# Optimization experiments

Measured on AMD Instinct MI355X. Metric: run time of the kernel, lower is better.

The kernel has to match this reference:

```python
import jax, jax.numpy as jnp
import numpy as np

B, C, H, W, NH = 4, 96, 256, 256, 4


def setup_inputs() -> dict:
    key = jax.random.key(0)
    ks = jax.random.split(key, 8)
    s = 0.05  # keep pre-activations well-scaled
    return {
        "x": jax.random.normal(ks[0], (B, C, H, W), jnp.float32),
        "ff": jax.random.normal(ks[1], (B, C, H, W), jnp.float32),
        "w_q": jax.random.normal(ks[2], (C, C, 1, 1), jnp.float32) * s,
        "w_kv": jax.random.normal(ks[3], (2 * C, C, 1, 1), jnp.float32) * s,
        "w_q_dw": jax.random.normal(ks[4], (C, 1, 3, 3), jnp.float32) * s,
        "w_kv_dw": jax.random.normal(ks[5], (2 * C, 1, 3, 3), jnp.float32) * s,
        "w_out": jax.random.normal(ks[6], (C, C, 1, 1), jnp.float32) * s,
        "temperature": jnp.ones((NH, 1, 1), jnp.float32),
    }


def _conv1x1(x, w):
    # pointwise conv == channel GEMM; w: [O, I, 1, 1]
    return jnp.einsum('bchw,oc->bohw', x, w[:, :, 0, 0])


def _dwconv3(x, w):
    # depthwise 3x3, padding=1; w: [C, 1, 3, 3]
    return jax.lax.conv_general_dilated(
        x, w, window_strides=(1, 1), padding='SAME',
        feature_group_count=x.shape[1],
        dimension_numbers=('NCHW', 'OIHW', 'NCHW'))


def _l2norm(t, eps=1e-12):
    # L2-normalize along last (HW) axis, torch F.normalize semantics
    n = jnp.sqrt(jnp.sum(t * t, axis=-1, keepdims=True))
    return t / jnp.maximum(n, eps)


def reference(x, ff, w_q, w_kv, w_q_dw, w_kv_dw, w_out, temperature):
    b, c, h, w = x.shape
    q = _dwconv3(_conv1x1(ff, w_q), w_q_dw)          # [B,C,H,W]
    kv = _dwconv3(_conv1x1(x, w_kv), w_kv_dw)        # [B,2C,H,W]
    k, v = jnp.split(kv, 2, axis=1)

    def heads(t):
        return t.reshape(b, NH, c // NH, h * w)       # [B,nh,c,HW]

    q = _l2norm(heads(q))
    k = _l2norm(heads(k))
    v = heads(v)
    # channel-wise (transposed) attention: [B,nh,c,c]
    attn = jax.nn.softmax(jnp.einsum('bhcn,bhdn->bhcd', q, k) * temperature, axis=-1)
    o = jnp.einsum('bhcd,bhdn->bhcn', attn, v).reshape(b, c, h, w)
    return _conv1x1(o, w_out)
```

## Files before the change

kernel.cpp:

```cpp
#include <hip/hip_runtime.h>
#include <hip/hip_bf16.h>
#include <hip/hip_fp16.h>

typedef unsigned int u32;
typedef unsigned short u16;
typedef _Float16 f16;

static constexpr int HWn = 65536;

typedef __attribute__((ext_vector_type(8))) f16 f16x8;
typedef __attribute__((ext_vector_type(4))) float f32x4;

__device__ __forceinline__ float h2f(u16 u) {
    union { u16 s; f16 h; } z; z.s = u; return (float)z.h;
}
__device__ __forceinline__ u16 f2h(float f) {
    union { u16 s; f16 h; } z; z.h = (f16)f; return z.s;
}
__device__ __forceinline__ u32 pack2h(float a, float b) {
    union { u32 i; f16 h[2]; } z; z.h[0] = (f16)a; z.h[1] = (f16)b; return z.i;
}
__device__ __forceinline__ float hlo(u32 u) {
    union { u32 i; f16 h[2]; } z; z.i = u; return (float)z.h[0];
}
__device__ __forceinline__ float hhi(u32 u) {
    union { u32 i; f16 h[2]; } z; z.i = u; return (float)z.h[1];
}
__device__ __forceinline__ float sq2h(u32 a) {
    const float l = hlo(a), h = hhi(a);
    return fmaf(l, l, h * h);
}

__device__ __forceinline__ int xoff(int px, int icb) {
    return px * 128 + (((icb ^ (px & 7) ^ ((px >> 3) & 7))) << 3);
}

__global__ __launch_bounds__(256) void k_prep_w(
    const float* __restrict__ wq, const float* __restrict__ wkv,
    u16* __restrict__ wf)
{
    const int i = blockIdx.x * 256 + threadIdx.x;
    if (i >= 288 * 96) return;
    const int row = i / 96, ic = i % 96;
    const float w = (row < 96) ? wq[row * 96 + ic] : wkv[(row - 96) * 96 + ic];
    wf[i] = f2h(w);
}

__global__ __launch_bounds__(256, 5) void k_conv_mfma(
    const float* __restrict__ ff, const float* __restrict__ x,
    const u16* __restrict__ wf,
    u16* __restrict__ qpre, u16* __restrict__ kvpre)
{
    const int b = blockIdx.z, sec = blockIdx.y;
    const int px0 = blockIdx.x * 128;
    const int tid = threadIdx.x;

    __shared__ __align__(16) u16 xs[16384];

    const float* src = (sec == 0 ? ff : x) + (size_t)b * 96 * HWn;

    const int icq = (tid >> 4) * 2;
    const int pxs = (tid & 15) * 8;
    #pragma unroll 1
    for (int p = 0; p < 3; ++p) {
        const int ic = p * 32 + icq;
        const float* rp0 = src + (size_t)ic * HWn + px0 + pxs;
        const float* rp1 = rp0 + HWn;
        const float4 a0 = *reinterpret_cast<const float4*>(rp0);
        const float4 a1 = *reinterpret_cast<const float4*>(rp0 + 4);
        const float4 b0 = *reinterpret_cast<const float4*>(rp1);
        const float4 b1 = *reinterpret_cast<const float4*>(rp1 + 4);
        const int icb = ic >> 3, icl = ic & 7;
        const float e0[8] = {a0.x, a0.y, a0.z, a0.w, a1.x, a1.y, a1.z, a1.w};
        const float e1[8] = {b0.x, b0.y, b0.z, b0.w, b1.x, b1.y, b1.z, b1.w};
        #pragma unroll
        for (int j = 0; j < 8; ++j) {
            const int o = xoff(pxs + j, icb) + icl;
            *reinterpret_cast<u32*>(&xs[o]) = pack2h(e0[j], e1[j]);
        }
    }
    __syncthreads();

    const int lane = tid & 63;
    const int wv = tid >> 6;
    const int oc0 = (wv >> 1) * 48;
    const int pxw = (wv & 1) * 64;
    const int lr = lane & 15, lg = lane >> 4;

    const int npass = (sec == 0) ? 1 : 2;
    #pragma unroll 1
    for (int kvs = 0; kvs < npass; ++kvs) {
        const u16* wh = wf + ((sec == 0) ? 0 : (96 + kvs * 96)) * 96;
        u16* dst = (sec == 0) ? (qpre + (size_t)b * 96 * HWn)
                              : (kvpre + (size_t)b * 192 * HWn + (size_t)kvs * 96 * HWn);

        f32x4 acc[3][4];
        #pragma unroll
        for (int m = 0; m < 3; ++m)
            #pragma unroll
            for (int n = 0; n < 4; ++n)
                acc[m][n] = (f32x4){0.f, 0.f, 0.f, 0.f};

        #pragma unroll 1
        for (int kt = 0; kt < 3; ++kt) {
            const int kb = kt * 32;
            f16x8 B[4];
            #pragma unroll
            for (int n = 0; n < 4; ++n)
                B[n] = *(const f16x8*)(xs + xoff(pxw + n * 16 + lr, (kb >> 3) + lg));
            f16x8 A[3];
            #pragma unroll
            for (int m = 0; m < 3; ++m)
                A[m] = *(const f16x8*)(wh + (oc0 + m * 16 + lr) * 96 + kb + lg * 8);
            #pragma unroll
            for (int m = 0; m < 3; ++m)
                #pragma unroll
                for (int n = 0; n < 4; ++n)
                    acc[m][n] = __builtin_amdgcn_mfma_f32_16x16x32_f16(A[m], B[n], acc[m][n], 0, 0, 0);
        }

        #pragma unroll
        for (int m = 0; m < 3; ++m) {
            #pragma unroll
            for (int i = 0; i < 4; ++i) {
                const int oc = oc0 + m * 16 + lg * 4 + i;
                u16* drow = dst + (size_t)oc * HWn + px0;
                #pragma unroll
                for (int n = 0; n < 4; ++n)
                    drow[pxw + n * 16 + lr] = f2h(acc[m][n][i]);
            }
        }
    }
}

__global__ __launch_bounds__(512) void k_dw_fused(
    const u16* __restrict__ qpre, const u16* __restrict__ kvpre,
    const float* __restrict__ wqdw, const float* __restrict__ wkvdw,
    u16* __restrict__ vout, float* __restrict__ ssq, float* __restrict__ Sg)
{
    const int bid = blockIdx.x;
    const int wg = (bid & 7) * 256 + (bid >> 3);
    const int b = wg >> 9;
    const int rem = wg & 511;
    const int y = rem >> 1;
    const int tx = (rem & 1) * 128;
    const int tid = threadIdx.x;
    const int lane = tid & 63;
    const int chunk = tid & 15;
    const int x0l = chunk * 8;
    const int xg = tx + x0l;

    __shared__ __align__(16) u16 qs[96][136];
    __shared__ __align__(16) u16 ks[96][136];

    #pragma unroll 1
    for (int it = 0; it < 9; ++it) {
        const int p = it * 32 + (tid >> 4);
        const u16* src; const float* wp; int c;
        if (p < 96)       { c = p;       src = qpre  + ((size_t)(b * 96 + c)) * HWn;       wp = wqdw  + c * 9; }
        else if (p < 192) { c = p - 96;  src = kvpre + ((size_t)(b * 192 + c)) * HWn;      wp = wkvdw + c * 9; }
        else              { c = p - 192; src = kvpre + ((size_t)(b * 192 + 96 + c)) * HWn; wp = wkvdw + (96 + c) * 9; }

        float a0 = 0.f, a1 = 0.f, a2 = 0.f, a3 = 0.f, a4 = 0.f, a5 = 0.f, a6 = 0.f, a7 = 0.f;

        #pragma unroll
        for (int r = 0; r < 3; ++r) {
            const int ry = y + r - 1;
            if ((unsigned)ry < 256u) {
                const u16* row = src + ry * 256 + xg;
                const uint4 m = *reinterpret_cast<const uint4*>(row);
                const float v1 = hlo(m.x), v2 = hhi(m.x);
                const float v3 = hlo(m.y), v4 = hhi(m.y);
                const float v5 = hlo(m.z), v6 = hhi(m.z);
                const float v7 = hlo(m.w), v8 = hhi(m.w);
                const float lv = __shfl(v8, (lane - 1) & 63);
                const float rv = __shfl(v1, (lane + 1) & 63);
                const float v0 = (chunk == 0)  ? ((xg > 0)       ? h2f(row[-1]) : 0.f) : lv;
                const float v9 = (chunk == 15) ? ((xg + 8 < 256) ? h2f(row[8])  : 0.f) : rv;
                const float w0 = wp[r * 3 + 0], w1 = wp[r * 3 + 1], w2 = wp[r * 3 + 2];
                a0 = fmaf(w0, v0, fmaf(w1, v1, fmaf(w2, v2, a0)));
                a1 = fmaf(w0, v1, fmaf(w1, v2, fmaf(w2, v3, a1)));
                a2 = fmaf(w0, v2, fmaf(w1, v3, fmaf(w2, v4, a2)));
                a3 = fmaf(w0, v3, fmaf(w1, v4, fmaf(w2, v5, a3)));
                a4 = fmaf(w0, v4, fmaf(w1, v5, fmaf(w2, v6, a4)));
                a5 = fmaf(w0, v5, fmaf(w1, v6, fmaf(w2, v7, a5)));
                a6 = fmaf(w0, v6, fmaf(w1, v7, fmaf(w2, v8, a6)));
                a7 = fmaf(w0, v7, fmaf(w1, v8, fmaf(w2, v9, a7)));
            }
        }

        const uint4 o = make_uint4(pack2h(a0, a1), pack2h(a2, a3), pack2h(a4, a5), pack2h(a6, a7));
        if (p < 96) {
            *reinterpret_cast<uint4*>(&qs[c][x0l]) = o;
        } else if (p < 192) {
            *reinterpret_cast<uint4*>(&ks[c][x0l]) = o;
        } else {
            *reinterpret_cast<uint4*>(vout + ((size_t)(b * 96 + c)) * HWn + y * 256 + xg) = o;
        }
    }
    __syncthreads();

    if (tid < 384) {
        const int half = tid >= 192;
        const int r = tid - half * 192;
        const uint4* rr = reinterpret_cast<const uint4*>(
            (r < 96 ? &qs[r][0] : &ks[r - 96][0]) + half * 64);
        float s = 0.f;
        #pragma unroll
        for (int pch = 0; pch < 8; ++pch) {
            const uint4 a = rr[pch];
            s += sq2h(a.x) + sq2h(a.y) + sq2h(a.z) + sq2h(a.w);
        }
        atomicAdd(ssq + b * 192 + r, s);
    }

    {
        const int w = tid >> 6;
        const int h = w & 3, mt = w >> 2;
        const int lr2 = lane & 15, lg2 = lane >> 4;
        const int ar = h * 24 + min(mt * 16 + lr2, 23);
        f32x4 acc2[2];
        acc2[0] = (f32x4){0.f, 0.f, 0.f, 0.f};
        acc2[1] = (f32x4){0.f, 0.f, 0.f, 0.f};
        #pragma unroll
        for (int ks4 = 0; ks4 < 4; ++ks4) {
            const f16x8 A = *(const f16x8*)(&qs[ar][ks4 * 32 + lg2 * 8]);
            #pragma unroll
            for (int nt = 0; nt < 2; ++nt) {
                const int bc = h * 24 + min(nt * 16 + lr2, 23);
                const f16x8 B = *(const f16x8*)(&ks[bc][ks4 * 32 + lg2 * 8]);
                acc2[nt] = __builtin_amdgcn_mfma_f32_16x16x32_f16(A, B, acc2[nt], 0, 0, 0);
            }
        }
        #pragma unroll
        for (int nt = 0; nt < 2; ++nt) {
            const int col = nt * 16 + lr2;
            #pragma unroll
            for (int reg = 0; reg < 4; ++reg) {
                const int row24 = mt * 16 + lg2 * 4 + reg;
                if (row24 < 24 && col < 24)
                    atomicAdd(Sg + b * 2304 + h * 576 + row24 * 24 + col, acc2[nt][reg]);
            }
        }
    }
}

__global__ __launch_bounds__(256) void k_attn_fold(
    const float* __restrict__ ssq, const float* __restrict__ S,
    const float* __restrict__ temp, const float* __restrict__ w_out,
    u16* __restrict__ mf)
{
    const int b = blockIdx.x;
    const int tid = threadIdx.x;
    __shared__ float rq[96], rk[96], att[2304];

    if (tid < 96) {
        rq[tid] = 1.f / fmaxf(sqrtf(ssq[b * 192 + tid]), 1e-12f);
    } else if (tid < 192) {
        const int c = tid - 96;
        rk[c] = 1.f / fmaxf(sqrtf(ssq[b * 192 + 96 + c]), 1e-12f);
    }
    __syncthreads();

    if (tid < 96) {
        const int h = tid / 24, i = tid % 24;
        const float tmp = temp[h];
        const float rqi = rq[h * 24 + i];
        float l[24];
        float m = -1e30f;
        #pragma unroll
        for (int j = 0; j < 24; ++j) {
            l[j] = S[b * 2304 + (h * 24 + i) * 24 + j] * rqi * rk[h * 24 + j] * tmp;
            m = fmaxf(m, l[j]);
        }
        float ssum = 0.f;
        #pragma unroll
        for (int j = 0; j < 24; ++j) { l[j] = expf(l[j] - m); ssum += l[j]; }
        const float inv = 1.f / ssum;
        #pragma unroll
        for (int j = 0; j < 24; ++j) att[(h * 24 + i) * 24 + j] = l[j] * inv;
    }
    __syncthreads();

    for (int k = 0; k < 36; ++k) {
        const int id = k * 256 + tid;
        const int dg = id / 96, oc = id % 96;
        const int h = dg / 24, d24 = dg % 24;
        float s = 0.f;
        #pragma unroll
        for (int i = 0; i < 24; ++i) {
            s += w_out[oc * 96 + h * 24 + i] * att[(h * 24 + i) * 24 + d24];
        }
        mf[b * 9216 + oc * 96 + dg] = f2h(s);
    }
}

__global__ __launch_bounds__(256, 5) void k_out_mfma(
    const u16* __restrict__ v, const u16* __restrict__ mf,
    float* __restrict__ out)
{
    const int b = blockIdx.y;
    const int px0 = blockIdx.x * 128;
    const int tid = threadIdx.x;
    __shared__ __align__(16) u16 xt[16384];

    const u16* vb = v + (size_t)b * 96 * HWn;
    const u16* mh = mf + b * 9216;

    const int icq = (tid >> 4) * 2;
    const int pxs = (tid & 15) * 8;
    #pragma unroll 1
    for (int p = 0; p < 3; ++p) {
        const int dg = p * 32 + icq;
        const uint4 u0 = *reinterpret_cast<const uint4*>(vb + (size_t)dg * HWn + px0 + pxs);
        const uint4 u1 = *reinterpret_cast<const uint4*>(vb + (size_t)(dg + 1) * HWn + px0 + pxs);
        const u32 w0[4] = {u0.x, u0.y, u0.z, u0.w};
        const u32 w1[4] = {u1.x, u1.y, u1.z, u1.w};
        const int icb = dg >> 3, icl = dg & 7;
        #pragma unroll
        for (int j = 0; j < 8; ++j) {
            const u32 lo = (w0[j >> 1] >> ((j & 1) * 16)) & 0xffffu;
            const u32 hi = (w1[j >> 1] >> ((j & 1) * 16)) & 0xffffu;
            const int o = xoff(pxs + j, icb) + icl;
            *reinterpret_cast<u32*>(&xt[o]) = (hi << 16) | lo;
        }
    }
    __syncthreads();

    const int lane = tid & 63;
    const int wv = tid >> 6;
    const int oc0 = (wv >> 1) * 48;
    const int pxw = (wv & 1) * 64;
    const int lr = lane & 15, lg = lane >> 4;

    f32x4 acc[3][4];
    #pragma unroll
    for (int m = 0; m < 3; ++m)
        #pragma unroll
        for (int n = 0; n < 4; ++n)
            acc[m][n] = (f32x4){0.f, 0.f, 0.f, 0.f};

    #pragma unroll 1
    for (int kt = 0; kt < 3; ++kt) {
        const int kb = kt * 32;
        f16x8 B[4];
        #pragma unroll
        for (int n = 0; n < 4; ++n)
            B[n] = *(const f16x8*)(xt + xoff(pxw + n * 16 + lr, (kb >> 3) + lg));
        f16x8 A[3];
        #pragma unroll
        for (int m = 0; m < 3; ++m)
            A[m] = *(const f16x8*)(mh + (oc0 + m * 16 + lr) * 96 + kb + lg * 8);
        #pragma unroll
        for (int m = 0; m < 3; ++m)
            #pragma unroll
            for (int n = 0; n < 4; ++n)
                acc[m][n] = __builtin_amdgcn_mfma_f32_16x16x32_f16(A[m], B[n], acc[m][n], 0, 0, 0);
    }

    #pragma unroll
    for (int m = 0; m < 3; ++m) {
        #pragma unroll
        for (int i = 0; i < 4; ++i) {
            const int oc = oc0 + m * 16 + lg * 4 + i;
            float* drow = out + ((size_t)(b * 96 + oc)) * HWn + px0;
            #pragma unroll
            for (int n = 0; n < 4; ++n)
                drow[pxw + n * 16 + lr] = acc[m][n][i];
        }
    }
}

extern "C" void kernel_launch(void* const* d_in, const int* in_sizes, int n_in,
                              void* d_out, int out_size, void* d_ws, size_t ws_size,
                              hipStream_t stream) {
    (void)in_sizes; (void)n_in; (void)out_size; (void)ws_size;
    const float* x      = (const float*)d_in[0];
    const float* ff     = (const float*)d_in[1];
    const float* w_q    = (const float*)d_in[2];
    const float* w_kv   = (const float*)d_in[3];
    const float* w_q_dw = (const float*)d_in[4];
    const float* w_kv_dw= (const float*)d_in[5];
    const float* w_out  = (const float*)d_in[6];
    const float* temp   = (const float*)d_in[7];
    float* out = (float*)d_out;

    char* ws = (char*)d_ws;
    u16* qpre   = (u16*)(ws);
    u16* kvpre  = (u16*)(ws + 50331648);
    u16* vbuf   = (u16*)(ws + 150994944);
    float* ssq  = (float*)(ws + 201326592);
    float* S    = (float*)(ws + 201329664);
    u16* wf     = (u16*)(ws + 201366528);
    u16* mf     = (u16*)(ws + 201421824);

    hipMemsetAsync(ssq, 0, 3072 + 36864, stream);

    k_prep_w<<<108, 256, 0, stream>>>(w_q, w_kv, wf);
    k_conv_mfma<<<dim3(512, 2, 4), 256, 0, stream>>>(ff, x, wf, qpre, kvpre);
    k_dw_fused<<<dim3(2048), 512, 0, stream>>>(qpre, kvpre, w_q_dw, w_kv_dw, vbuf, ssq, S);
    k_attn_fold<<<4, 256, 0, stream>>>(ssq, S, temp, w_out, mf);
    k_out_mfma<<<dim3(512, 4), 256, 0, stream>>>(vbuf, mf, out);
}
```

Before: 275.4 us.

## Prefetch depthwise rows, spread atomic reductions over partial copies, unroll staging loops

The depthwise kernel now issues the global loads for the next channel before computing the current one, with boundary handling folded into predicated loads. This is meant to hide load latency. Atomic accumulation of squared norms and Q·K scores is spread across 32 partial buffers indexed by block, to cut contention on the same addresses. The attention-fold kernel then sums those partials. Load-staging loops in the conv and output kernels are also fully unrolled. The trade-off is higher register pressure, a larger memset, and extra reduction work in the fold kernel.

```diff
diff --git a/kernel.cpp b/kernel.cpp
--- a/kernel.cpp
+++ b/kernel.cpp
@@ -7,6 +7,7 @@
 typedef _Float16 f16;
 
 static constexpr int HWn = 65536;
+static constexpr int NCOPY = 32;
 
 typedef __attribute__((ext_vector_type(8))) f16 f16x8;
 typedef __attribute__((ext_vector_type(4))) float f32x4;
@@ -61,7 +62,7 @@
 
     const int icq = (tid >> 4) * 2;
     const int pxs = (tid & 15) * 8;
-    #pragma unroll 1
+    #pragma unroll
     for (int p = 0; p < 3; ++p) {
         const int ic = p * 32 + icq;
         const float* rp0 = src + (size_t)ic * HWn + px0 + pxs;
@@ -133,69 +134,106 @@
     }
 }
 
+__device__ __forceinline__ void dw_addr(
+    int it, int pq, int b,
+    const u16* qpre, const u16* kvpre, const float* wqdw, const float* wkvdw,
+    const u16*& src, const float*& wp, int& c, int& seg)
+{
+    const int p = it * 32 + pq;
+    if (p < 96)       { c = p;       src = qpre  + ((size_t)(b * 96 + c)) * HWn;       wp = wqdw  + c * 9; seg = 0; }
+    else if (p < 192) { c = p - 96;  src = kvpre + ((size_t)(b * 192 + c)) * HWn;      wp = wkvdw + c * 9; seg = 1; }
+    else              { c = p - 192; src = kvpre + ((size_t)(b * 192 + 96 + c)) * HWn; wp = wkvdw + (96 + c) * 9; seg = 2; }
+}
+
 __global__ __launch_bounds__(512) void k_dw_fused(
     const u16* __restrict__ qpre, const u16* __restrict__ kvpre,
     const float* __restrict__ wqdw, const float* __restrict__ wkvdw,
-    u16* __restrict__ vout, float* __restrict__ ssq, float* __restrict__ Sg)
+    u16* __restrict__ vout, float* __restrict__ ssqp, float* __restrict__ Spart)
 {
     const int bid = blockIdx.x;
     const int wg = (bid & 7) * 256 + (bid >> 3);
+    const int copy = bid & (NCOPY - 1);
     const int b = wg >> 9;
     const int rem = wg & 511;
     const int y = rem >> 1;
     const int tx = (rem & 1) * 128;
     const int tid = threadIdx.x;
     const int lane = tid & 63;
+    const int pq = tid >> 4;
     const int chunk = tid & 15;
     const int x0l = chunk * 8;
     const int xg = tx + x0l;
 
+    const bool vr0 = (y > 0), vr2 = (y < 255);
+    const bool le = (chunk == 0) && (xg > 0);
+    const bool re = (chunk == 15) && (xg + 8 < 256);
+
     __shared__ __align__(16) u16 qs[96][136];
     __shared__ __align__(16) u16 ks[96][136];
 
+    auto issue = [&](const u16* src, uint4* m, u32* el, u32* er) {
+        const uint4 z = make_uint4(0u, 0u, 0u, 0u);
+        const u16* r0 = src + (y - 1) * 256 + xg;
+        const u16* r1 = r0 + 256;
+        const u16* r2 = r1 + 256;
+        m[0] = vr0 ? *reinterpret_cast<const uint4*>(r0) : z;
+        m[1] = *reinterpret_cast<const uint4*>(r1);
+        m[2] = vr2 ? *reinterpret_cast<const uint4*>(r2) : z;
+        el[0] = (le && vr0) ? r0[-1] : 0u;  er[0] = (re && vr0) ? r0[8] : 0u;
+        el[1] = le ? r1[-1] : 0u;           er[1] = re ? r1[8] : 0u;
+        el[2] = (le && vr2) ? r2[-1] : 0u;  er[2] = (re && vr2) ? r2[8] : 0u;
+    };
+
+    const u16* srcC; const float* wpC; int cC, segC;
+    dw_addr(0, pq, b, qpre, kvpre, wqdw, wkvdw, srcC, wpC, cC, segC);
+    uint4 mcur[3]; u32 elc[3], erc[3];
+    issue(srcC, mcur, elc, erc);
+
     #pragma unroll 1
     for (int it = 0; it < 9; ++it) {
-        const int p = it * 32 + (tid >> 4);
-        const u16* src; const float* wp; int c;
-        if (p < 96)       { c = p;       src = qpre  + ((size_t)(b * 96 + c)) * HWn;       wp = wqdw  + c * 9; }
-        else if (p < 192) { c = p - 96;  src = kvpre + ((size_t)(b * 192 + c)) * HWn;      wp = wkvdw + c * 9; }
-        else              { c = p - 192; src = kvpre + ((size_t)(b * 192 + 96 + c)) * HWn; wp = wkvdw + (96 + c) * 9; }
+        const u16* srcN; const float* wpN; int cN, segN;
+        uint4 mnx[3]; u32 eln[3], ern[3];
+        if (it < 8) {
+            dw_addr(it + 1, pq, b, qpre, kvpre, wqdw, wkvdw, srcN, wpN, cN, segN);
+            issue(srcN, mnx, eln, ern);
+        }
 
         float a0 = 0.f, a1 = 0.f, a2 = 0.f, a3 = 0.f, a4 = 0.f, a5 = 0.f, a6 = 0.f, a7 = 0.f;
-
         #pragma unroll
         for (int r = 0; r < 3; ++r) {
-            const int ry = y + r - 1;
-            if ((unsigned)ry < 256u) {
-                const u16* row = src + ry * 256 + xg;
-                const uint4 m = *reinterpret_cast<const uint4*>(row);
-                const float v1 = hlo(m.x), v2 = hhi(m.x);
-                const float v3 = hlo(m.y), v4 = hhi(m.y);
-                const float v5 = hlo(m.z), v6 = hhi(m.z);
-                const float v7 = hlo(m.w), v8 = hhi(m.w);
-                const float lv = __shfl(v8, (lane - 1) & 63);
-                const float rv = __shfl(v1, (lane + 1) & 63);
-                const float v0 = (chunk == 0)  ? ((xg > 0)       ? h2f(row[-1]) : 0.f) : lv;
-                const float v9 = (chunk == 15) ? ((xg + 8 < 256) ? h2f(row[8])  : 0.f) : rv;
-                const float w0 = wp[r * 3 + 0], w1 = wp[r * 3 + 1], w2 = wp[r * 3 + 2];
-                a0 = fmaf(w0, v0, fmaf(w1, v1, fmaf(w2, v2, a0)));
-                a1 = fmaf(w0, v1, fmaf(w1, v2, fmaf(w2, v3, a1)));
-                a2 = fmaf(w0, v2, fmaf(w1, v3, fmaf(w2, v4, a2)));
-                a3 = fmaf(w0, v3, fmaf(w1, v4, fmaf(w2, v5, a3)));
-                a4 = fmaf(w0, v4, fmaf(w1, v5, fmaf(w2, v6, a4)));
-                a5 = fmaf(w0, v5, fmaf(w1, v6, fmaf(w2, v7, a5)));
-                a6 = fmaf(w0, v6, fmaf(w1, v7, fmaf(w2, v8, a6)));
-                a7 = fmaf(w0, v7, fmaf(w1, v8, fmaf(w2, v9, a7)));
-            }
+            const uint4 m = mcur[r];
+            const float v1 = hlo(m.x), v2 = hhi(m.x);
+            const float v3 = hlo(m.y), v4 = hhi(m.y);
+            const float v5 = hlo(m.z), v6 = hhi(m.z);
+            const float v7 = hlo(m.w), v8 = hhi(m.w);
+            const float lv = __shfl(v8, (lane - 1) & 63);
+            const float rv = __shfl(v1, (lane + 1) & 63);
+            const float v0 = (chunk == 0)  ? h2f((u16)elc[r]) : lv;
+            const float v9 = (chunk == 15) ? h2f((u16)erc[r]) : rv;
+            const float w0 = wpC[r * 3 + 0], w1 = wpC[r * 3 + 1], w2 = wpC[r * 3 + 2];
+            a0 = fmaf(w0, v0, fmaf(w1, v1, fmaf(w2, v2, a0)));
+            a1 = fmaf(w0, v1, fmaf(w1, v2, fmaf(w2, v3, a1)));
+            a2 = fmaf(w0, v2, fmaf(w1, v3, fmaf(w2, v4, a2)));
+            a3 = fmaf(w0, v3, fmaf(w1, v4, fmaf(w2, v5, a3)));
+            a4 = fmaf(w0, v4, fmaf(w1, v5, fmaf(w2, v6, a4)));
+            a5 = fmaf(w0, v5, fmaf(w1, v6, fmaf(w2, v7, a5)));
+            a6 = fmaf(w0, v6, fmaf(w1, v7, fmaf(w2, v8, a6)));
+            a7 = fmaf(w0, v7, fmaf(w1, v8, fmaf(w2, v9, a7)));
         }
 
         const uint4 o = make_uint4(pack2h(a0, a1), pack2h(a2, a3), pack2h(a4, a5), pack2h(a6, a7));
-        if (p < 96) {
-            *reinterpret_cast<uint4*>(&qs[c][x0l]) = o;
-        } else if (p < 192) {
-            *reinterpret_cast<uint4*>(&ks[c][x0l]) = o;
+        if (segC == 0) {
+            *reinterpret_cast<uint4*>(&qs[cC][x0l]) = o;
+        } else if (segC == 1) {
+            *reinterpret_cast<uint4*>(&ks[cC][x0l]) = o;
         } else {
-            *reinterpret_cast<uint4*>(vout + ((size_t)(b * 96 + c)) * HWn + y * 256 + xg) = o;
+            *reinterpret_cast<uint4*>(vout + ((size_t)(b * 96 + cC)) * HWn + y * 256 + xg) = o;
+        }
+
+        if (it < 8) {
+            #pragma unroll
+            for (int r = 0; r < 3; ++r) { mcur[r] = mnx[r]; elc[r] = eln[r]; erc[r] = ern[r]; }
+            wpC = wpN; cC = cN; segC = segN;
         }
     }
     __syncthreads();
@@ -211,7 +249,7 @@
             const uint4 a = rr[pch];
             s += sq2h(a.x) + sq2h(a.y) + sq2h(a.z) + sq2h(a.w);
         }
-        atomicAdd(ssq + b * 192 + r, s);
+        atomicAdd(ssqp + (copy * 4 + b) * 192 + r, s);
     }
 
     {
@@ -232,6 +270,7 @@
                 acc2[nt] = __builtin_amdgcn_mfma_f32_16x16x32_f16(A, B, acc2[nt], 0, 0, 0);
             }
         }
+        float* Sdst = Spart + (copy * 4 + b) * 2304 + h * 576;
         #pragma unroll
         for (int nt = 0; nt < 2; ++nt) {
             const int col = nt * 16 + lr2;
@@ -239,14 +278,14 @@
             for (int reg = 0; reg < 4; ++reg) {
                 const int row24 = mt * 16 + lg2 * 4 + reg;
                 if (row24 < 24 && col < 24)
-                    atomicAdd(Sg + b * 2304 + h * 576 + row24 * 24 + col, acc2[nt][reg]);
+                    atomicAdd(Sdst + row24 * 24 + col, acc2[nt][reg]);
             }
         }
     }
 }
 
 __global__ __launch_bounds__(256) void k_attn_fold(
-    const float* __restrict__ ssq, const float* __restrict__ S,
+    const float* __restrict__ Spart, const float* __restrict__ ssqp,
     const float* __restrict__ temp, const float* __restrict__ w_out,
     u16* __restrict__ mf)
 {
@@ -254,11 +293,18 @@
     const int tid = threadIdx.x;
     __shared__ float rq[96], rk[96], att[2304];
 
-    if (tid < 96) {
-        rq[tid] = 1.f / fmaxf(sqrtf(ssq[b * 192 + tid]), 1e-12f);
-    } else if (tid < 192) {
-        const int c = tid - 96;
-        rk[c] = 1.f / fmaxf(sqrtf(ssq[b * 192 + 96 + c]), 1e-12f);
+    for (int v = tid; v < 2304; v += 256) {
+        float s = 0.f;
+        #pragma unroll 4
+        for (int cp = 0; cp < NCOPY; ++cp) s += Spart[(cp * 4 + b) * 2304 + v];
+        att[v] = s;
+    }
+    if (tid < 192) {
+        float s = 0.f;
+        #pragma unroll 4
+        for (int cp = 0; cp < NCOPY; ++cp) s += ssqp[(cp * 4 + b) * 192 + tid];
+        const float r = 1.f / fmaxf(sqrtf(s), 1e-12f);
+        if (tid < 96) rq[tid] = r; else rk[tid - 96] = r;
     }
     __syncthreads();
 
@@ -270,7 +316,7 @@
         float m = -1e30f;
         #pragma unroll
         for (int j = 0; j < 24; ++j) {
-            l[j] = S[b * 2304 + (h * 24 + i) * 24 + j] * rqi * rk[h * 24 + j] * tmp;
+            l[j] = att[(h * 24 + i) * 24 + j] * rqi * rk[h * 24 + j] * tmp;
             m = fmaxf(m, l[j]);
         }
         float ssum = 0.f;
@@ -309,7 +355,7 @@
 
     const int icq = (tid >> 4) * 2;
     const int pxs = (tid & 15) * 8;
-    #pragma unroll 1
+    #pragma unroll
     for (int p = 0; p < 3; ++p) {
         const int dg = p * 32 + icq;
         const uint4 u0 = *reinterpret_cast<const uint4*>(vb + (size_t)dg * HWn + px0 + pxs);
@@ -389,16 +435,16 @@
     u16* qpre   = (u16*)(ws);
     u16* kvpre  = (u16*)(ws + 50331648);
     u16* vbuf   = (u16*)(ws + 150994944);
-    float* ssq  = (float*)(ws + 201326592);
-    float* S    = (float*)(ws + 201329664);
-    u16* wf     = (u16*)(ws + 201366528);
-    u16* mf     = (u16*)(ws + 201421824);
-
-    hipMemsetAsync(ssq, 0, 3072 + 36864, stream);
+    float* Spart= (float*)(ws + 201326592);
+    float* ssqp = (float*)(ws + 202506240);
+    u16* wf     = (u16*)(ws + 202604544);
+    u16* mf     = (u16*)(ws + 202659840);
+
+    hipMemsetAsync(ws + 201326592, 0, 1179648 + 98304, stream);
 
     k_prep_w<<<108, 256, 0, stream>>>(w_q, w_kv, wf);
     k_conv_mfma<<<dim3(512, 2, 4), 256, 0, stream>>>(ff, x, wf, qpre, kvpre);
-    k_dw_fused<<<dim3(2048), 512, 0, stream>>>(qpre, kvpre, w_q_dw, w_kv_dw, vbuf, ssq, S);
-    k_attn_fold<<<4, 256, 0, stream>>>(ssq, S, temp, w_out, mf);
+    k_dw_fused<<<dim3(2048), 512, 0, stream>>>(qpre, kvpre, w_q_dw, w_kv_dw, vbuf, ssqp, Spart);
+    k_attn_fold<<<4, 256, 0, stream>>>(Spart, ssqp, temp, w_out, mf);
     k_out_mfma<<<dim3(512, 4), 256, 0, stream>>>(vbuf, mf, out);
 }
```

New measurement: 306.7 us. 1.11x slower.
